# Kernel tuning notes

Measured on AMD Instinct MI355X. Metric: run time of the kernel, lower is better.

Reference implementation:

```python
import jax, jax.numpy as jnp
import numpy as np

B, R, D = 16, 2048, 512
H2, NREL = 2 * D, 2048  # relation_mlp hidden = 2*d_model, output = n_relations
MIN_PROB = 0.1          # early-stop probability threshold from the torch code


def setup_inputs() -> dict:
    key = jax.random.key(0)
    ks = jax.random.split(key, 8)
    sc = lambda k, shp: jax.random.normal(k, shp, jnp.float32) * 0.02
    return {
        "rel_encoding": jax.random.normal(ks[0], (B, R, D), jnp.float32),
        "na_emb": jax.random.normal(ks[1], (D,), jnp.float32),
        "v_w": sc(ks[2], (D, D)), "v_b": jnp.zeros((D,), jnp.float32),
        "o_w": sc(ks[3], (D, D)), "o_b": jnp.zeros((D,), jnp.float32),
        "ln_g": jnp.ones((D,), jnp.float32), "ln_b": jnp.zeros((D,), jnp.float32),
        "w1": sc(ks[4], (H2, D)), "b1": jnp.zeros((H2,), jnp.float32),
        "w2": sc(ks[5], (NREL, H2)), "b2": jnp.zeros((NREL,), jnp.float32),
    }


def _ln(x, g, b, eps=1e-5):
    m = jnp.mean(x, axis=-1, keepdims=True)
    v = jnp.var(x, axis=-1, keepdims=True)
    return (x - m) * jax.lax.rsqrt(v + eps) * g + b


def reference(rel_encoding, na_emb, v_w, v_b, o_w, o_b, ln_g, ln_b, w1, b1, w2, b2):
    # Cross-attention with a single key/value token: softmax over a length-1 axis
    # is identically 1, so attn_out = out_proj(v_proj(kv)) for every query position.
    x = rel_encoding                                         # [B,R,D]
    attn = (x @ v_w.T + v_b) @ o_w.T + o_b                   # [B,R,D]

    def step_logits(state):                                  # state broadcasts to [B,R,D]
        h = _ln(attn + state, ln_g, ln_b)                    # residual + layernorm
        return jax.nn.relu(h @ w1.T + b1) @ w2.T + b2        # [B,R,NREL]

    # step 0: query is the na_embedding
    p0 = jax.nn.softmax(step_logits(na_emb), axis=-1)
    m0 = jnp.max(p0, axis=-1)
    i0 = jnp.argmax(p0, axis=-1)
    cont0 = (i0 != 0) & (m0 >= MIN_PROB)                     # else break before step 0 emits

    # step 1: last appended state is the relation encoding itself
    p1 = jax.nn.softmax(step_logits(x), axis=-1)
    m1 = jnp.max(p1, axis=-1)
    i1 = jnp.argmax(p1, axis=-1)
    cont1 = cont0 & (i1 != 0) & (m1 >= MIN_PROB)

    # rule_score = prod of accepted step probs; 0.0 if no step accepted
    scores = jnp.where(cont0, jnp.where(cont1, m0 * m1, m0), 0.0)  # [B,R]
    lengths = cont0.astype(jnp.int32) + cont1.astype(jnp.int32)    # ragged rule lengths
    return scores, i0, i1, lengths
```

## Files before the change

### kernel.cpp

```cpp
#include <hip/hip_runtime.h>
#include <math.h>

#define MTOT 32768
#define DD   512
#define HHD  1024
#define NRELN 2048
#define SCA  64.f
#define SCB  1024.f
#define INVS (1.f / 65536.f)
#define CAPR 4096
#define MARGIN 2.0e-3f

typedef _Float16 h8  __attribute__((ext_vector_type(8)));
typedef float    f4  __attribute__((ext_vector_type(4)));
typedef float    f16v __attribute__((ext_vector_type(16)));

__device__ __forceinline__ void fsplit(float x, _Float16& h, _Float16& l) {
  _Float16 t = (_Float16)x;
  h = t;
  l = (_Float16)(x - (float)t);
}

__device__ __forceinline__ void gld16(const _Float16* g, _Float16* l) {
  __builtin_amdgcn_global_load_lds(
      (const __attribute__((address_space(1))) void*)g,
      (__attribute__((address_space(3))) void*)l, 16, 0, 0);
}


__global__ void prep_wvo_split(const float* __restrict__ vw, const float* __restrict__ ow,
                               _Float16* __restrict__ wh, _Float16* __restrict__ wl) {
  int idx = blockIdx.x * 256 + threadIdx.x;
  int k = idx & 511;
  int n = idx >> 9;
  float s = 0.f;
  for (int j = 0; j < DD; ++j) s += ow[n * DD + j] * vw[j * DD + k];
  fsplit(s * SCB, wh[n * DD + k], wl[n * DD + k]);
}

__global__ void prep_cvec(const float* __restrict__ ow, const float* __restrict__ vb,
                          const float* __restrict__ ob, float* __restrict__ c) {
  int i = blockIdx.x * 256 + threadIdx.x;
  if (i < DD) {
    float s = ob[i];
    for (int k = 0; k < DD; ++k) s += ow[i * DD + k] * vb[k];
    c[i] = s;
  }
}

__global__ void prep_w1p_split(const float* __restrict__ w1, const float* __restrict__ g,
                               _Float16* __restrict__ wh, _Float16* __restrict__ wl) {
  int idx = blockIdx.x * 256 + threadIdx.x;
  int k = idx & 511;
  int n = idx >> 9;
  fsplit(w1[n * DD + k] * g[k] * SCB, wh[n * DD + k], wl[n * DD + k]);
}

__global__ void prep_b1p(const float* __restrict__ w1, const float* __restrict__ lnb,
                         const float* __restrict__ b1, float* __restrict__ b1p) {
  int n = blockIdx.x * 256 + threadIdx.x;
  if (n < HHD) {
    float s = b1[n];
    for (int k = 0; k < DD; ++k) s += w1[n * DD + k] * lnb[k];
    b1p[n] = s;
  }
}

__global__ void prep_w2_split(const float* __restrict__ w2,
                              _Float16* __restrict__ wh, _Float16* __restrict__ wl) {
  int idx = blockIdx.x * 256 + threadIdx.x;
  int k = idx & 1023;
  int n = idx >> 10;
  fsplit(w2[n * HHD + k] * SCB, wh[n * HHD + k], wl[n * HHD + k]);
}

__global__ void split_x(const float* __restrict__ src, _Float16* __restrict__ h,
                        _Float16* __restrict__ l) {
  int idx = (blockIdx.x * 256 + threadIdx.x) * 8;
  float4 a = *(const float4*)(src + idx);
  float4 b = *(const float4*)(src + idx + 4);
  float vv[8] = {a.x, a.y, a.z, a.w, b.x, b.y, b.z, b.w};
  _Float16 hh[8], ll[8];
#pragma unroll
  for (int i = 0; i < 8; ++i) fsplit(vv[i] * SCA, hh[i], ll[i]);
  *(h8*)(h + idx) = *(h8*)hh;
  *(h8*)(l + idx) = *(h8*)ll;
}

__global__ void zero_cnt(int* c) { c[blockIdx.x * 256 + threadIdx.x] = 0; }

template <int MODE, int KDIM, int NTOT>
__global__ __launch_bounds__(256) void gemm_split(
    const _Float16* __restrict__ Ah, const _Float16* __restrict__ Al,
    const _Float16* __restrict__ Bh, const _Float16* __restrict__ Bl,
    const float* __restrict__ bias,
    float* __restrict__ outF,
    _Float16* __restrict__ outHh, _Float16* __restrict__ outHl,
    float* __restrict__ pM, float* __restrict__ pI,
    const int* __restrict__ cntp, int pstr) {
  __shared__ __align__(16) _Float16 sA[2][128][32];
  __shared__ __align__(16) _Float16 sB[2][128][32];
  const int t = threadIdx.x;
  const int lane = t & 63;
  const int wv = t >> 6;
  const int wr = wv & 1, wc = wv >> 1;
  const int l31 = lane & 31, half = lane >> 5;
  const int n0 = blockIdx.y << 7;

  const _Float16* gsp = (wv == 0) ? Ah : (wv == 1) ? Al : (wv == 2) ? Bh : Bl;
  _Float16* lbase = (wv == 0) ? &sA[0][0][0] : (wv == 1) ? &sA[1][0][0]
                  : (wv == 2) ? &sB[0][0][0] : &sB[1][0][0];
  const int srow = lane >> 2;
  const int scp = lane & 3;
  const int swzE = ((srow >> 1) & 3) ^ ((srow >> 3) & 1);
  const int swzO = swzE ^ 2;
  const int swz = ((l31 >> 1) ^ (l31 >> 3)) & 3;

  int nmb;
  if constexpr (MODE == 2) {
    int a = *cntp;
    if (a > CAPR) a = CAPR;
    nmb = (a + 127) >> 7;
  } else {
    nmb = gridDim.x;
  }

  for (int mb = blockIdx.x; mb < nmb; mb += gridDim.x) {
    const int m0 = mb << 7;
    const int gb = (wv < 2) ? m0 : n0;
    const _Float16* gA0 = gsp + (size_t)(gb + srow) * KDIM + ((scp ^ swzE) << 3);
    const _Float16* gA1 = gsp + (size_t)(gb + srow) * KDIM + ((scp ^ swzO) << 3);

    f16v acc[2][2] = {};
    for (int k0 = 0; k0 < KDIM; k0 += 32) {
      __syncthreads();
#pragma unroll
      for (int it = 0; it < 8; ++it)
        gld16(((it & 1) ? gA1 : gA0) + (size_t)(it * 16) * KDIM + k0, lbase + it * 512);
      __syncthreads();
#pragma unroll
      for (int ks = 0; ks < 2; ++ks) {
        const int pos = (((ks << 1) + half) ^ swz) << 3;
        h8 af_h[2], af_l[2], bf_h[2], bf_l[2];
#pragma unroll
        for (int i = 0; i < 2; ++i) {
          const int mr = wr * 64 + i * 32 + l31;
          af_h[i] = *(const h8*)&sA[0][mr][pos];
          af_l[i] = *(const h8*)&sA[1][mr][pos];
        }
#pragma unroll
        for (int j = 0; j < 2; ++j) {
          const int nr = wc * 64 + j * 32 + l31;
          bf_h[j] = *(const h8*)&sB[0][nr][pos];
          bf_l[j] = *(const h8*)&sB[1][nr][pos];
        }
#pragma unroll
        for (int j = 0; j < 2; ++j)
#pragma unroll
          for (int i = 0; i < 2; ++i) {
            acc[i][j] = __builtin_amdgcn_mfma_f32_32x32x16_f16(af_h[i], bf_h[j], acc[i][j], 0, 0, 0);
            acc[i][j] = __builtin_amdgcn_mfma_f32_32x32x16_f16(af_h[i], bf_l[j], acc[i][j], 0, 0, 0);
            acc[i][j] = __builtin_amdgcn_mfma_f32_32x32x16_f16(af_l[i], bf_h[j], acc[i][j], 0, 0, 0);
          }
      }
    }

    float bb[2];
    int gc[2];
#pragma unroll
    for (int j = 0; j < 2; ++j) {
      gc[j] = n0 + wc * 64 + j * 32 + l31;
      bb[j] = bias[gc[j]];
    }
    if constexpr (MODE == 0) {
#pragma unroll
      for (int i = 0; i < 2; ++i)
#pragma unroll
        for (int r = 0; r < 16; ++r) {
          const int row = m0 + wr * 64 + i * 32 + (r & 3) + 8 * (r >> 2) + 4 * half;
#pragma unroll
          for (int j = 0; j < 2; ++j)
            outF[(size_t)row * NTOT + gc[j]] = acc[i][j][r] * INVS + bb[j];
        }
    } else if constexpr (MODE == 1) {
#pragma unroll
      for (int i = 0; i < 2; ++i)
#pragma unroll
        for (int r = 0; r < 16; ++r) {
          const int row = m0 + wr * 64 + i * 32 + (r & 3) + 8 * (r >> 2) + 4 * half;
#pragma unroll
          for (int j = 0; j < 2; ++j) {
            float v = fmaxf(acc[i][j][r] * INVS + bb[j], 0.f) * SCA;
            _Float16 hh, ll;
            fsplit(v, hh, ll);
            outHh[(size_t)row * NTOT + gc[j]] = hh;
            outHl[(size_t)row * NTOT + gc[j]] = ll;
          }
        }
    } else {
      const int slot = blockIdx.y * 2 + wc;
#pragma unroll
      for (int i = 0; i < 2; ++i)
#pragma unroll
        for (int r = 0; r < 16; ++r) {
          float v0 = acc[i][0][r] * INVS + bb[0];
          float v1 = acc[i][1][r] * INVS + bb[1];
          float M;
          int I;
          if (v0 >= v1) { M = v0; I = gc[0]; }
          else          { M = v1; I = gc[1]; }
#pragma unroll
          for (int sh = 1; sh <= 16; sh <<= 1) {
            float M2 = __shfl_xor(M, sh);
            int   I2 = __shfl_xor(I, sh);
            if (M2 > M || (M2 == M && I2 < I)) { M = M2; I = I2; }
          }
          if (l31 == 0) {
            const int grow = m0 + wr * 64 + i * 32 + (r & 3) + 8 * (r >> 2) + 4 * half;
            pM[(size_t)slot * pstr + grow] = M;
            pI[(size_t)slot * pstr + grow] = (float)I;
          }
        }
    }
  }
}

__global__ __launch_bounds__(256) void gemm_approx(
    const _Float16* __restrict__ Ah, const _Float16* __restrict__ Bh,
    const float* __restrict__ bias,
    float* __restrict__ pM, float* __restrict__ pM2,
    float* __restrict__ pS, int* __restrict__ pI, int astr) {
  __shared__ __align__(16) _Float16 sAll[8192];
  const int t = threadIdx.x;
  const int lane = t & 63;
  const int wv = t >> 6;
  const int wr = wv & 1, wc = wv >> 1;
  const int q = lane >> 4, l16 = lane & 15;
  const int nb = blockIdx.x * 2 + (blockIdx.y & 1);
  const int mb = blockIdx.y >> 1;
  const int m0 = mb << 7;
  const int n0 = nb << 7;

  const _Float16* src0[4];
#pragma unroll
  for (int it = 0; it < 4; ++it) {
    int p = it * 256 + t;
    int row = (p & 511) >> 2;
    int cp = p & 3;
    int sw = ((row >> 1) ^ (row >> 3)) & 3;
    const _Float16* base = (p < 512) ? (Ah + (size_t)(m0 + row) * HHD)
                                     : (Bh + (size_t)(n0 + row) * HHD);
    src0[it] = base + ((cp ^ sw) << 3);
  }
  _Float16* dstw = sAll + (size_t)(wv * 64) * 8;

  int offA[4], offB[4];
#pragma unroll
  for (int i = 0; i < 4; ++i) {
    int ra = wr * 64 + i * 16 + l16;
    int swa = ((ra >> 1) ^ (ra >> 3)) & 3;
    offA[i] = ra * 32 + ((q ^ swa) << 3);
    int rb = wc * 64 + i * 16 + l16;
    int swb = ((rb >> 1) ^ (rb >> 3)) & 3;
    offB[i] = 4096 + rb * 32 + ((q ^ swb) << 3);
  }

  f4 acc[4][4] = {};
  for (int k0 = 0; k0 < HHD; k0 += 32) {
    __syncthreads();
#pragma unroll
    for (int it = 0; it < 4; ++it)
      gld16(src0[it] + k0, dstw + it * 2048);
    __syncthreads();
    h8 af[4], bf[4];
#pragma unroll
    for (int i = 0; i < 4; ++i) af[i] = *(const h8*)&sAll[offA[i]];
#pragma unroll
    for (int j = 0; j < 4; ++j) bf[j] = *(const h8*)&sAll[offB[j]];
#pragma unroll
    for (int j = 0; j < 4; ++j)
#pragma unroll
      for (int i = 0; i < 4; ++i)
        acc[i][j] = __builtin_amdgcn_mfma_f32_16x16x32_f16(af[i], bf[j], acc[i][j], 0, 0, 0);
  }

  const int slot = nb * 2 + wc;
  float bb[4];
  int gc[4];
#pragma unroll
  for (int j = 0; j < 4; ++j) {
    gc[j] = n0 + wc * 64 + j * 16 + l16;
    bb[j] = bias[gc[j]];
  }
#pragma unroll
  for (int i = 0; i < 4; ++i)
#pragma unroll
    for (int rr = 0; rr < 4; ++rr) {
      float M = acc[i][0][rr] * INVS + bb[0], M2 = -INFINITY, S = 1.f;
      int I = gc[0];
#pragma unroll
      for (int j = 1; j < 4; ++j) {
        float v = acc[i][j][rr] * INVS + bb[j];
        if (v > M || (v == M && gc[j] < I)) {
          S = S * __expf(M - v) + 1.f; M2 = M; M = v; I = gc[j];
        } else {
          S += __expf(v - M); M2 = fmaxf(M2, v);
        }
      }
#pragma unroll
      for (int sh = 1; sh <= 8; sh <<= 1) {
        float Mo = __shfl_xor(M, sh);
        float M2o = __shfl_xor(M2, sh);
        float So = __shfl_xor(S, sh);
        int   Io = __shfl_xor(I, sh);
        if (Mo > M || (Mo == M && Io < I)) {
          S = S * __expf(M - Mo) + So; M2 = fmaxf(M, M2o); M = Mo; I = Io;
        } else {
          S += So * __expf(Mo - M); M2 = fmaxf(M2, Mo);
        }
      }
      if (l16 == 0) {
        const int grow = m0 + wr * 64 + i * 16 + q * 4 + rr;
        pM[(size_t)slot * astr + grow] = M;
        pM2[(size_t)slot * astr + grow] = M2;
        pS[(size_t)slot * astr + grow] = S;
        pI[(size_t)slot * astr + grow] = I;
      }
    }
}

__global__ void flag_k(const float* __restrict__ pM, const float* __restrict__ pM2,
                       const float* __restrict__ pS, const int* __restrict__ pI,
                       int astr, int rows,
                       float* __restrict__ map, int* __restrict__ iap, int row0,
                       int* __restrict__ list, int* __restrict__ cnt) {
  int r = blockIdx.x * 256 + threadIdx.x;
  if (r >= rows) return;
  float M = pM[r], M2 = pM2[r], S = pS[r];
  int I = pI[r];
  for (int s = 1; s < 32; ++s) {
    size_t o = (size_t)s * astr + r;
    float m = pM[o], m2 = pM2[o], ss = pS[o];
    int ii = pI[o];
    if (m > M || (m == M && ii < I)) {
      M2 = fmaxf(M, m2); S = S * __expf(M - m) + ss; M = m; I = ii;
    } else {
      M2 = fmaxf(M2, m); S += ss * __expf(m - M);
    }
  }
  map[row0 + r] = 1.f / S;
  iap[row0 + r] = I;
  if (M - M2 < MARGIN) {
    int c = atomicAdd(cnt, 1);
    if (c < CAPR) list[c] = r;
  }
}

__global__ void gather_k(const _Float16* __restrict__ Hh, const _Float16* __restrict__ Hl,
                         const int* __restrict__ list, const int* __restrict__ cnt,
                         _Float16* __restrict__ Gh, _Float16* __restrict__ Gl) {
  int b = blockIdx.x;
  int active = *cnt;
  if (active > CAPR) active = CAPR;
  if (b >= active) return;
  int r = list[b];
  int t = threadIdx.x;
  *(h8*)(Gh + (size_t)b * HHD + t * 8) = *(const h8*)(Hh + (size_t)r * HHD + t * 8);
  *(h8*)(Gl + (size_t)b * HHD + t * 8) = *(const h8*)(Hl + (size_t)r * HHD + t * 8);
}

__global__ void rescue_merge(const float* __restrict__ pMr, const float* __restrict__ pIr,
                             const int* __restrict__ list, const int* __restrict__ cnt,
                             int* __restrict__ iap, int row0) {
  int c = blockIdx.x * 256 + threadIdx.x;
  int a = *cnt;
  if (a > CAPR) a = CAPR;
  if (c >= a) return;
  float M = pMr[c];
  int I = (int)pIr[c];
  for (int s = 1; s < 32; ++s) {
    size_t o = (size_t)s * CAPR + c;
    float m = pMr[o];
    int i2 = (int)pIr[o];
    if (m > M || (m == M && i2 < I)) { M = m; I = i2; }
  }
  iap[row0 + list[c]] = I;
}

__global__ __launch_bounds__(256) void ln_dual(
    const float* __restrict__ A, const float* __restrict__ X,
    const float* __restrict__ na,
    _Float16* __restrict__ y0h, _Float16* __restrict__ y0l,
    _Float16* __restrict__ y1h, _Float16* __restrict__ y1l) {
  int t = threadIdx.x;
  int lane = t & 63;
  int w = t >> 6;
  int r = blockIdx.x * 4 + w;
  const float* ap = A + (size_t)r * DD + lane * 8;
  const float* xp = X + (size_t)r * DD + lane * 8;
  const float* np = na + lane * 8;
  float v0[8], v1[8];
  float s0 = 0.f, q0 = 0.f, s1 = 0.f, q1 = 0.f;
#pragma unroll
  for (int i = 0; i < 8; ++i) {
    float a = ap[i];
    v0[i] = a + np[i];
    v1[i] = a + xp[i];
    s0 += v0[i]; q0 += v0[i] * v0[i];
    s1 += v1[i]; q1 += v1[i] * v1[i];
  }
#pragma unroll
  for (int m = 1; m <= 32; m <<= 1) {
    s0 += __shfl_xor(s0, m); q0 += __shfl_xor(q0, m);
    s1 += __shfl_xor(s1, m); q1 += __shfl_xor(q1, m);
  }
  float mu0 = s0 * (1.f / DD), mu1 = s1 * (1.f / DD);
  float rs0 = 1.f / sqrtf(q0 * (1.f / DD) - mu0 * mu0 + 1e-5f);
  float rs1 = 1.f / sqrtf(q1 * (1.f / DD) - mu1 * mu1 + 1e-5f);
  _Float16 h0[8], l0[8], h1[8], l1[8];
#pragma unroll
  for (int i = 0; i < 8; ++i) {
    fsplit((v0[i] - mu0) * rs0 * SCA, h0[i], l0[i]);
    fsplit((v1[i] - mu1) * rs1 * SCA, h1[i], l1[i]);
  }
  *(h8*)(y0h + (size_t)r * DD + lane * 8) = *(h8*)h0;
  *(h8*)(y0l + (size_t)r * DD + lane * 8) = *(h8*)l0;
  *(h8*)(y1h + (size_t)r * DD + lane * 8) = *(h8*)h1;
  *(h8*)(y1l + (size_t)r * DD + lane * 8) = *(h8*)l1;
}

__global__ void finalize_k(const float* __restrict__ map0, const int* __restrict__ iap0,
                           const float* __restrict__ map1, const int* __restrict__ iap1,
                           float* __restrict__ out) {
  int r = blockIdx.x * 256 + threadIdx.x;
  float m0v = map0[r], m1v = map1[r];
  int i0v = iap0[r], i1v = iap1[r];
  bool c0 = (i0v != 0) && (m0v >= 0.1f);
  bool c1 = c0 && (i1v != 0) && (m1v >= 0.1f);
  out[r] = c0 ? (c1 ? m0v * m1v : m0v) : 0.f;
  out[MTOT + r] = (float)i0v;
  out[2 * MTOT + r] = (float)i1v;
  out[3 * MTOT + r] = (float)((c0 ? 1 : 0) + (c1 ? 1 : 0));
}

extern "C" void kernel_launch(void* const* d_in, const int* in_sizes, int n_in,
                              void* d_out, int out_size, void* d_ws, size_t ws_size,
                              hipStream_t stream) {
  const float* X   = (const float*)d_in[0];
  const float* na  = (const float*)d_in[1];
  const float* vw  = (const float*)d_in[2];
  const float* vb  = (const float*)d_in[3];
  const float* ow  = (const float*)d_in[4];
  const float* ob  = (const float*)d_in[5];
  const float* lng = (const float*)d_in[6];
  const float* lnb = (const float*)d_in[7];
  const float* w1  = (const float*)d_in[8];
  const float* b1  = (const float*)d_in[9];
  const float* w2  = (const float*)d_in[10];
  const float* b2  = (const float*)d_in[11];
  float* out = (float*)d_out;

  char* p = (char*)d_ws;
  auto alloc = [&](size_t bytes) -> void* {
    void* r = (void*)p;
    p += (bytes + 255) & ~(size_t)255;
    return r;
  };
  _Float16* wvo_h = (_Float16*)alloc(512 * 512 * 2);
  _Float16* wvo_l = (_Float16*)alloc(512 * 512 * 2);
  float*    cvec  = (float*)alloc(512 * 4);
  _Float16* w1p_h = (_Float16*)alloc(1024 * 512 * 2);
  _Float16* w1p_l = (_Float16*)alloc(1024 * 512 * 2);
  float*    b1p   = (float*)alloc(1024 * 4);
  _Float16* w2_h  = (_Float16*)alloc(2048 * 1024 * 2);
  _Float16* w2_l  = (_Float16*)alloc(2048 * 1024 * 2);
  float* map0 = (float*)alloc((size_t)MTOT * 4);
  float* map1 = (float*)alloc((size_t)MTOT * 4);
  int* iap0 = (int*)alloc((size_t)MTOT * 4);
  int* iap1 = (int*)alloc((size_t)MTOT * 4);
  int* list = (int*)alloc(CAPR * 4);
  int* cnt  = (int*)alloc(512 * 4);
  float* pMr = (float*)alloc((size_t)32 * CAPR * 4);
  float* pIr = (float*)alloc((size_t)32 * CAPR * 4);
  _Float16* Gh = (_Float16*)alloc((size_t)CAPR * HHD * 2);
  _Float16* Gl = (_Float16*)alloc((size_t)CAPR * HHD * 2);

  size_t fixed = (size_t)(p - (char*)d_ws);
  size_t reserve = 2u << 20;
  size_t remain = ws_size > fixed + reserve ? ws_size - fixed - reserve : 0;
  int chunk = (int)(remain / 10752);
  chunk &= ~127;
  if (chunk < 128) chunk = 128;
  if (chunk > MTOT) chunk = MTOT;

  _Float16* xs_h = (_Float16*)alloc((size_t)chunk * 512 * 2);
  _Float16* xs_l = (_Float16*)alloc((size_t)chunk * 512 * 2);
  float*    Abuf = (float*)alloc((size_t)chunk * 512 * 4);
  _Float16* y0_h = (_Float16*)alloc((size_t)chunk * 512 * 2);
  _Float16* y0_l = (_Float16*)alloc((size_t)chunk * 512 * 2);
  _Float16* H_h  = (_Float16*)alloc((size_t)chunk * 1024 * 2);
  _Float16* H_l  = (_Float16*)alloc((size_t)chunk * 1024 * 2);
  float* pMa  = (float*)alloc((size_t)32 * chunk * 4);
  float* pM2a = (float*)alloc((size_t)32 * chunk * 4);
  float* pSa  = (float*)alloc((size_t)32 * chunk * 4);
  int*   pIa  = (int*)alloc((size_t)32 * chunk * 4);
  _Float16* y1_h = xs_h;
  _Float16* y1_l = xs_l;

  zero_cnt<<<2, 256, 0, stream>>>(cnt);
  prep_wvo_split<<<1024, 256, 0, stream>>>(vw, ow, wvo_h, wvo_l);
  prep_cvec<<<2, 256, 0, stream>>>(ow, vb, ob, cvec);
  prep_w1p_split<<<2048, 256, 0, stream>>>(w1, lng, w1p_h, w1p_l);
  prep_b1p<<<4, 256, 0, stream>>>(w1, lnb, b1, b1p);
  prep_w2_split<<<8192, 256, 0, stream>>>(w2, w2_h, w2_l);

  int citer = 0;
  for (int row0 = 0; row0 < MTOT; row0 += chunk, ++citer) {
    int rows = (MTOT - row0 < chunk) ? (MTOT - row0) : chunk;
    split_x<<<rows * 512 / 2048, 256, 0, stream>>>(X + (size_t)row0 * 512, xs_h, xs_l);
    gemm_split<0, 512, 512><<<dim3(rows / 128, 4), 256, 0, stream>>>(
        xs_h, xs_l, wvo_h, wvo_l, cvec, Abuf, nullptr, nullptr,
        nullptr, nullptr, nullptr, 0);
    ln_dual<<<rows / 4, 256, 0, stream>>>(Abuf, X + (size_t)row0 * 512, na,
                                          y0_h, y0_l, y1_h, y1_l);
    for (int s = 0; s < 2; ++s) {
      int* cp = cnt + citer * 2 + s;
      gemm_split<1, 512, 1024><<<dim3(rows / 128, 8), 256, 0, stream>>>(
          s == 0 ? y0_h : y1_h, s == 0 ? y0_l : y1_l, w1p_h, w1p_l, b1p,
          nullptr, H_h, H_l, nullptr, nullptr, nullptr, 0);
      gemm_approx<<<dim3(8, (rows / 128) * 2), 256, 0, stream>>>(
          H_h, w2_h, b2, pMa, pM2a, pSa, pIa, chunk);
      flag_k<<<(rows + 255) / 256, 256, 0, stream>>>(
          pMa, pM2a, pSa, pIa, chunk, rows,
          s == 0 ? map0 : map1, s == 0 ? iap0 : iap1, row0, list, cp);
      gather_k<<<CAPR, 128, 0, stream>>>(H_h, H_l, list, cp, Gh, Gl);
      gemm_split<2, 1024, 2048><<<dim3(32, 16), 256, 0, stream>>>(
          Gh, Gl, w2_h, w2_l, b2, nullptr, nullptr, nullptr,
          pMr, pIr, cp, CAPR);
      rescue_merge<<<CAPR / 256, 256, 0, stream>>>(
          pMr, pIr, list, cp, s == 0 ? iap0 : iap1, row0);
    }
  }
  finalize_k<<<MTOT / 256, 256, 0, stream>>>(map0, iap0, map1, iap1, out);
}
```

Baseline: 1.477 ms.

## Widen gemm_approx tile to 128x256 and remap blocks for grouped scheduling

The approximate logits GEMM now computes a 128x256 output tile per block (8 B fragments per wave) instead of 128x128, with the block grid remapped so groups of M-blocks share an N-slice. This raises arithmetic intensity per LDS load and halves the number of partial softmax slots that flag_k must merge (16 instead of 32). Chunk size is rounded to multiples of 1024 rows to keep the grouping even. The cost is higher register pressure from the 4x8 accumulators, which launch_bounds(256,2) constrains and which may cause spilling.

```diff
diff --git a/kernel.cpp b/kernel.cpp
--- a/kernel.cpp
+++ b/kernel.cpp
@@ -225,71 +225,73 @@
   }
 }
 
-__global__ __launch_bounds__(256) void gemm_approx(
+__global__ __launch_bounds__(256, 2) void gemm_approx(
     const _Float16* __restrict__ Ah, const _Float16* __restrict__ Bh,
     const float* __restrict__ bias,
     float* __restrict__ pM, float* __restrict__ pM2,
-    float* __restrict__ pS, int* __restrict__ pI, int astr) {
-  __shared__ __align__(16) _Float16 sAll[8192];
+    float* __restrict__ pS, int* __restrict__ pI, int astr, int mpg) {
+  __shared__ __align__(16) _Float16 sAll[12288];
   const int t = threadIdx.x;
   const int lane = t & 63;
   const int wv = t >> 6;
   const int wr = wv & 1, wc = wv >> 1;
   const int q = lane >> 4, l16 = lane & 15;
-  const int nb = blockIdx.x * 2 + (blockIdx.y & 1);
-  const int mb = blockIdx.y >> 1;
+  const int nb = blockIdx.y / mpg;
+  const int mb = blockIdx.x * mpg + (blockIdx.y % mpg);
   const int m0 = mb << 7;
-  const int n0 = nb << 7;
-
-  const _Float16* src0[4];
-#pragma unroll
-  for (int it = 0; it < 4; ++it) {
+  const int n0 = nb << 8;
+
+  const _Float16* src0[6];
+#pragma unroll
+  for (int it = 0; it < 6; ++it) {
     int p = it * 256 + t;
-    int row = (p & 511) >> 2;
-    int cp = p & 3;
+    int row, cp;
+    const _Float16* base;
+    if (p < 512) { row = p >> 2; cp = p & 3; base = Ah + (size_t)(m0 + row) * HHD; }
+    else { int pq = p - 512; row = pq >> 2; cp = pq & 3; base = Bh + (size_t)(n0 + row) * HHD; }
     int sw = ((row >> 1) ^ (row >> 3)) & 3;
-    const _Float16* base = (p < 512) ? (Ah + (size_t)(m0 + row) * HHD)
-                                     : (Bh + (size_t)(n0 + row) * HHD);
     src0[it] = base + ((cp ^ sw) << 3);
   }
-  _Float16* dstw = sAll + (size_t)(wv * 64) * 8;
-
-  int offA[4], offB[4];
+
+  int offA[4], offB[8];
 #pragma unroll
   for (int i = 0; i < 4; ++i) {
     int ra = wr * 64 + i * 16 + l16;
     int swa = ((ra >> 1) ^ (ra >> 3)) & 3;
     offA[i] = ra * 32 + ((q ^ swa) << 3);
-    int rb = wc * 64 + i * 16 + l16;
+  }
+#pragma unroll
+  for (int j = 0; j < 8; ++j) {
+    int rb = wc * 128 + j * 16 + l16;
     int swb = ((rb >> 1) ^ (rb >> 3)) & 3;
-    offB[i] = 4096 + rb * 32 + ((q ^ swb) << 3);
-  }
-
-  f4 acc[4][4] = {};
+    offB[j] = 4096 + rb * 32 + ((q ^ swb) << 3);
+  }
+
+  f4 acc[4][8] = {};
   for (int k0 = 0; k0 < HHD; k0 += 32) {
     __syncthreads();
 #pragma unroll
-    for (int it = 0; it < 4; ++it)
-      gld16(src0[it] + k0, dstw + it * 2048);
+    for (int it = 0; it < 6; ++it)
+      gld16(src0[it] + k0, sAll + (it * 4 + wv) * 512);
     __syncthreads();
-    h8 af[4], bf[4];
+    h8 af[4], bf[8];
 #pragma unroll
     for (int i = 0; i < 4; ++i) af[i] = *(const h8*)&sAll[offA[i]];
 #pragma unroll
-    for (int j = 0; j < 4; ++j) bf[j] = *(const h8*)&sAll[offB[j]];
-#pragma unroll
-    for (int j = 0; j < 4; ++j)
+    for (int j = 0; j < 8; ++j) bf[j] = *(const h8*)&sAll[offB[j]];
+#pragma unroll
+    for (int j = 0; j < 8; ++j)
 #pragma unroll
       for (int i = 0; i < 4; ++i)
         acc[i][j] = __builtin_amdgcn_mfma_f32_16x16x32_f16(af[i], bf[j], acc[i][j], 0, 0, 0);
   }
 
   const int slot = nb * 2 + wc;
-  float bb[4];
-  int gc[4];
-#pragma unroll
-  for (int j = 0; j < 4; ++j) {
-    gc[j] = n0 + wc * 64 + j * 16 + l16;
+  float bb[8];
+  int gc[8];
+#pragma unroll
+  for (int j = 0; j < 8; ++j) {
+    gc[j] = n0 + wc * 128 + j * 16 + l16;
     bb[j] = bias[gc[j]];
   }
 #pragma unroll
@@ -299,7 +301,7 @@
       float M = acc[i][0][rr] * INVS + bb[0], M2 = -INFINITY, S = 1.f;
       int I = gc[0];
 #pragma unroll
-      for (int j = 1; j < 4; ++j) {
+      for (int j = 1; j < 8; ++j) {
         float v = acc[i][j][rr] * INVS + bb[j];
         if (v > M || (v == M && gc[j] < I)) {
           S = S * __expf(M - v) + 1.f; M2 = M; M = v; I = gc[j];
@@ -338,7 +340,7 @@
   if (r >= rows) return;
   float M = pM[r], M2 = pM2[r], S = pS[r];
   int I = pI[r];
-  for (int s = 1; s < 32; ++s) {
+  for (int s = 1; s < 16; ++s) {
     size_t o = (size_t)s * astr + r;
     float m = pM[o], m2 = pM2[o], ss = pS[o];
     int ii = pI[o];
@@ -488,9 +490,9 @@
   size_t fixed = (size_t)(p - (char*)d_ws);
   size_t reserve = 2u << 20;
   size_t remain = ws_size > fixed + reserve ? ws_size - fixed - reserve : 0;
-  int chunk = (int)(remain / 10752);
-  chunk &= ~127;
-  if (chunk < 128) chunk = 128;
+  int chunk = (int)(remain / 10496);
+  chunk &= ~1023;
+  if (chunk < 1024) chunk = 1024;
   if (chunk > MTOT) chunk = MTOT;
 
   _Float16* xs_h = (_Float16*)alloc((size_t)chunk * 512 * 2);
@@ -500,10 +502,10 @@
   _Float16* y0_l = (_Float16*)alloc((size_t)chunk * 512 * 2);
   _Float16* H_h  = (_Float16*)alloc((size_t)chunk * 1024 * 2);
   _Float16* H_l  = (_Float16*)alloc((size_t)chunk * 1024 * 2);
-  float* pMa  = (float*)alloc((size_t)32 * chunk * 4);
-  float* pM2a = (float*)alloc((size_t)32 * chunk * 4);
-  float* pSa  = (float*)alloc((size_t)32 * chunk * 4);
-  int*   pIa  = (int*)alloc((size_t)32 * chunk * 4);
+  float* pMa  = (float*)alloc((size_t)16 * chunk * 4);
+  float* pM2a = (float*)alloc((size_t)16 * chunk * 4);
+  float* pSa  = (float*)alloc((size_t)16 * chunk * 4);
+  int*   pIa  = (int*)alloc((size_t)16 * chunk * 4);
   _Float16* y1_h = xs_h;
   _Float16* y1_l = xs_l;
 
@@ -517,19 +519,20 @@
   int citer = 0;
   for (int row0 = 0; row0 < MTOT; row0 += chunk, ++citer) {
     int rows = (MTOT - row0 < chunk) ? (MTOT - row0) : chunk;
+    int mblocks = rows / 128;
     split_x<<<rows * 512 / 2048, 256, 0, stream>>>(X + (size_t)row0 * 512, xs_h, xs_l);
-    gemm_split<0, 512, 512><<<dim3(rows / 128, 4), 256, 0, stream>>>(
+    gemm_split<0, 512, 512><<<dim3(mblocks, 4), 256, 0, stream>>>(
         xs_h, xs_l, wvo_h, wvo_l, cvec, Abuf, nullptr, nullptr,
         nullptr, nullptr, nullptr, 0);
     ln_dual<<<rows / 4, 256, 0, stream>>>(Abuf, X + (size_t)row0 * 512, na,
                                           y0_h, y0_l, y1_h, y1_l);
     for (int s = 0; s < 2; ++s) {
       int* cp = cnt + citer * 2 + s;
-      gemm_split<1, 512, 1024><<<dim3(rows / 128, 8), 256, 0, stream>>>(
+      gemm_split<1, 512, 1024><<<dim3(mblocks, 8), 256, 0, stream>>>(
           s == 0 ? y0_h : y1_h, s == 0 ? y0_l : y1_l, w1p_h, w1p_l, b1p,
           nullptr, H_h, H_l, nullptr, nullptr, nullptr, 0);
-      gemm_approx<<<dim3(8, (rows / 128) * 2), 256, 0, stream>>>(
-          H_h, w2_h, b2, pMa, pM2a, pSa, pIa, chunk);
+      gemm_approx<<<dim3(8, mblocks), 256, 0, stream>>>(
+          H_h, w2_h, b2, pMa, pM2a, pSa, pIa, chunk, mblocks / 8);
       flag_k<<<(rows + 255) / 256, 256, 0, stream>>>(
           pMa, pM2a, pSa, pIa, chunk, rows,
           s == 0 ? map0 : map1, s == 0 ? iap0 : iap1, row0, list, cp);
```

New measurement: 1.484 ms. About the same (+0.5%).
